# Kernel optimization log

Hardware: AMD Instinct MI355X
Metric: run time of the kernel (lower is better)

## Reference

```python
import jax, jax.numpy as jnp
import numpy as np

MARGIN = 1.0

def setup_inputs() -> dict:
    key = jax.random.key(0)
    k1, k2 = jax.random.split(key)
    B, D, NUM_CLASSES = 4096, 512, 64
    inputs = jax.random.normal(k1, (B, D), dtype=jnp.float32)
    labels = jax.random.randint(k2, (B,), 0, NUM_CLASSES, dtype=jnp.int64)
    return {"inputs": inputs, "labels": labels}

def reference(inputs, labels):
    # Full pairwise squared L2 distances via the ||a-b||^2 = ||a||^2 + ||b||^2 - 2 a.b expansion
    sq = jnp.sum(inputs * inputs, axis=1)                      # [B]
    d2 = sq[:, None] + sq[None, :] - 2.0 * (inputs @ inputs.T)  # [B, B]
    d2 = jnp.maximum(d2, 0.0)
    # Safe sqrt: zero (self) distances get exactly 0 without NaN-producing sqrt(0) grads
    nz = d2 > 1e-12
    dist = jnp.where(nz, jnp.sqrt(jnp.where(nz, d2, 1.0)), 0.0)  # [B, B]

    mask = labels[:, None] == labels[None, :]                   # [B, B] same-class mask (includes self)
    mask_f = mask.astype(dist.dtype)

    # Per-anchor: mean distance to positives (self included, contributing 0, as in the torch loop)
    ap_mean = jnp.sum(dist * mask_f, axis=1) / jnp.sum(mask_f, axis=1)  # [B]
    # Per-anchor: min distance to negatives
    an_min = jnp.min(jnp.where(mask, jnp.inf, dist), axis=1)            # [B]

    tmp = ap_mean - an_min + MARGIN                             # [B]
    # `if tmp > 0: loss += tmp` over the batch == sum of relu(tmp)
    return jnp.sum(jnp.maximum(tmp, 0.0))
```

## Files before the change

kernel.cpp:

```cpp
#include <hip/hip_runtime.h>
#include <hip/hip_bf16.h>

typedef unsigned char u8;
typedef unsigned short u16;
typedef unsigned int u32;
typedef unsigned long long u64;
typedef __attribute__((ext_vector_type(4))) float f32x4;

#define B_SZ 4096
#define D_SZ 512
#define NCLS 64
#define BK   64
#define NKK  (D_SZ / BK)
#define NT   32
#define NBLK (NT * (NT + 1) / 2)
#define TILE_BYTES (128 * BK)

#define WAITV2()  asm volatile("s_waitcnt vmcnt(2)" ::: "memory")
#define WAITV0()  asm volatile("s_waitcnt vmcnt(0)" ::: "memory")
#define BARRIER() asm volatile("s_barrier" ::: "memory")


__device__ __forceinline__ u8 f2fp8(float x) {
    union { float f; u32 u; } a; a.f = x;
    u32 s = (a.u >> 24) & 0x80u;
    u32 m = a.u & 0x7fffffffu;
    u32 r = m + 0x7ffffu + ((m >> 20) & 1u);
    int e = (int)(r >> 23) - 127 + 7;
    u32 mant = (r >> 20) & 7u;
    if (e <= 0) return (u8)s;
    if (e >= 16) return (u8)(s | 0x7Eu);
    return (u8)(s | ((u32)e << 3) | mant);
}

__device__ __forceinline__ void gload16(const void* g, void* l) {
    __builtin_amdgcn_global_load_lds(
        (const __attribute__((address_space(1))) u32*)g,
        (__attribute__((address_space(3))) u32*)l,
        16, 0, 0);
}

__device__ __forceinline__ void stage_fp8(const u8* __restrict__ gsrc, u8* dst, int t) {
    const int r = t >> 2;
    const int c16 = (t & 3) ^ (r & 3);
    gload16(gsrc + (size_t)r * D_SZ + (c16 << 4), dst + t * 16);
}


__global__ __launch_bounds__(256) void prep_kernel(
    const float* __restrict__ in, u8* __restrict__ bf8,
    float* __restrict__ sq, float* __restrict__ ap_sum, u32* __restrict__ an_min)
{
    const int wave = threadIdx.x >> 6, l = threadIdx.x & 63;
    const int row = blockIdx.x * 4 + wave;
    const float* p = in + (size_t)row * D_SZ + l * 8;
    float4 v0 = *(const float4*)p;
    float4 v1 = *(const float4*)(p + 4);
    float s = v0.x*v0.x + v0.y*v0.y + v0.z*v0.z + v0.w*v0.w
            + v1.x*v1.x + v1.y*v1.y + v1.z*v1.z + v1.w*v1.w;
    u64 pk =  (u64)f2fp8(v0.x)
           | ((u64)f2fp8(v0.y) << 8)
           | ((u64)f2fp8(v0.z) << 16)
           | ((u64)f2fp8(v0.w) << 24)
           | ((u64)f2fp8(v1.x) << 32)
           | ((u64)f2fp8(v1.y) << 40)
           | ((u64)f2fp8(v1.z) << 48)
           | ((u64)f2fp8(v1.w) << 56);
    *(u64*)(bf8 + (size_t)row * D_SZ + l * 8) = pk;
    #pragma unroll
    for (int off = 1; off < 64; off <<= 1) s += __shfl_xor(s, off);
    if (l == 0) {
        sq[row] = s;
        ap_sum[row] = 0.0f;
        an_min[row] = 0x7f800000u;
    }
}


__global__ __launch_bounds__(512, 4) void tile_kernel(
    const u8* __restrict__ bf8, const int* __restrict__ lab,
    const float* __restrict__ sq, float* __restrict__ ap_sum, u32* __restrict__ an_min)
{
    __shared__ u8 As[3][TILE_BYTES];
    __shared__ u8 Bs[3][TILE_BYTES];
    __shared__ float sqA[128], sqB[128];
    __shared__ int labA[128], labB[128];

    const int t = threadIdx.x;

    int bid = blockIdx.x;
    bid = (bid & 7) * (NBLK / 8) + (bid >> 3);

    int tm = (int)((__builtin_sqrtf(8.0f * (float)bid + 1.0f) - 1.0f) * 0.5f);
    while ((tm + 1) * (tm + 2) / 2 <= bid) ++tm;
    while (tm * (tm + 1) / 2 > bid) --tm;
    const int tn = bid - tm * (tm + 1) / 2;
    const bool diag = (tm == tn);

    const int rowBase = tm * 128;
    const int colBase = tn * 128;

    if (t < 128) { labA[t] = lab[rowBase + t]; sqA[t] = sq[rowBase + t]; }
    else if (t < 256) { int u = t - 128; labB[u] = lab[colBase + u]; sqB[u] = sq[colBase + u]; }

    const int wave = t >> 6, lane = t & 63;
    const int wr = wave >> 1, wc = wave & 1;
    const int g = lane >> 4, c = lane & 15;

    f32x4 acc[2][4];
    #pragma unroll
    for (int i = 0; i < 2; ++i)
        #pragma unroll
        for (int j = 0; j < 4; ++j)
            acc[i][j] = (f32x4){0.f, 0.f, 0.f, 0.f};

    const u8* gA = bf8 + (size_t)rowBase * D_SZ;
    const u8* gB = bf8 + (size_t)colBase * D_SZ;

    __syncthreads();

    stage_fp8(gA,      As[0], t);
    stage_fp8(gB,      Bs[0], t);
    stage_fp8(gA + BK, As[1], t);
    stage_fp8(gB + BK, Bs[1], t);

    const int x3 = c & 3, sub = (g & 1) * 8, gh = g >> 1;

    #pragma unroll
    for (int kk = 0; kk < NKK; ++kk) {
        if (kk < NKK - 1) { WAITV2(); }
        else              { WAITV0(); }
        BARRIER();

        if (kk + 2 < NKK) {
            stage_fp8(gA + (kk + 2) * BK, As[(kk + 2) % 3], t);
            stage_fp8(gB + (kk + 2) * BK, Bs[(kk + 2) % 3], t);
        }

        const u8* abuf = As[kk % 3];
        const u8* bbuf = Bs[kk % 3];

        #pragma unroll
        for (int ks = 0; ks < 2; ++ks) {
            const int koff = (((ks * 2 + gh) ^ x3) << 4) + sub;
            long a[2], b[4];
            #pragma unroll
            for (int mi = 0; mi < 2; ++mi)
                a[mi] = *(const long*)(abuf + (wr * 32 + mi * 16 + c) * BK + koff);
            #pragma unroll
            for (int ni = 0; ni < 4; ++ni)
                b[ni] = *(const long*)(bbuf + (wc * 64 + ni * 16 + c) * BK + koff);
            #pragma unroll
            for (int mi = 0; mi < 2; ++mi)
                #pragma unroll
                for (int ni = 0; ni < 4; ++ni)
                    acc[mi][ni] = __builtin_amdgcn_mfma_f32_16x16x32_fp8_fp8(a[mi], b[ni], acc[mi][ni], 0, 0, 0);
        }
    }

    float sc[4], mc[4];
    #pragma unroll
    for (int ni = 0; ni < 4; ++ni) { sc[ni] = 0.0f; mc[ni] = __builtin_inff(); }

    #pragma unroll
    for (int mi = 0; mi < 2; ++mi) {
        #pragma unroll
        for (int r = 0; r < 4; ++r) {
            const int lrow = wr * 32 + mi * 16 + g * 4 + r;
            const int i = rowBase + lrow;
            const int li = labA[lrow];
            const float sqi = sqA[lrow];
            float s = 0.0f;
            float mn = __builtin_inff();
            #pragma unroll
            for (int ni = 0; ni < 4; ++ni) {
                const int lcol = wc * 64 + ni * 16 + c;
                float d2 = sqi + sqB[lcol] - 2.0f * acc[mi][ni][r];
                d2 = fmaxf(d2, 0.0f);
                float dist = (d2 > 1e-12f) ? __builtin_sqrtf(d2) : 0.0f;
                if (diag && lrow == lcol) dist = 0.0f;
                if (li == labB[lcol]) { s += dist; sc[ni] += dist; }
                else                  { mn = fminf(mn, dist); mc[ni] = fminf(mc[ni], dist); }
            }
            #pragma unroll
            for (int off = 1; off < 16; off <<= 1) {
                s += __shfl_xor(s, off);
                mn = fminf(mn, __shfl_xor(mn, off));
            }
            if (c == 0) {
                atomicAdd(&ap_sum[i], s);
                atomicMin(&an_min[i], __float_as_uint(mn));
            }
        }
    }

    if (!diag) {
        #pragma unroll
        for (int ni = 0; ni < 4; ++ni) {
            float s = sc[ni], mn = mc[ni];
            s += __shfl_xor(s, 16); s += __shfl_xor(s, 32);
            mn = fminf(mn, __shfl_xor(mn, 16)); mn = fminf(mn, __shfl_xor(mn, 32));
            if (lane < 16) {
                const int j = colBase + wc * 64 + ni * 16 + c;
                atomicAdd(&ap_sum[j], s);
                atomicMin(&an_min[j], __float_as_uint(mn));
            }
        }
    }
}


__global__ __launch_bounds__(1024) void final_kernel(
    const float* __restrict__ ap_sum, const u32* __restrict__ an_min,
    const int* __restrict__ lab, float* __restrict__ out)
{
    __shared__ int cnt[NCLS];
    __shared__ float wsum[16];
    const int t = threadIdx.x;
    if (t < NCLS) cnt[t] = 0;
    __syncthreads();
    for (int i = t; i < B_SZ; i += 1024) atomicAdd(&cnt[lab[i]], 1);
    __syncthreads();
    float v = 0.0f;
    for (int i = t; i < B_SZ; i += 1024) {
        float apm = ap_sum[i] / (float)cnt[lab[i]];
        float anm = __uint_as_float(an_min[i]);
        v += fmaxf(apm - anm + 1.0f, 0.0f);
    }
    #pragma unroll
    for (int off = 1; off < 64; off <<= 1) v += __shfl_xor(v, off);
    if ((t & 63) == 0) wsum[t >> 6] = v;
    __syncthreads();
    if (t == 0) {
        float s = 0.0f;
        #pragma unroll
        for (int w = 0; w < 16; ++w) s += wsum[w];
        out[0] = s;
    }
}


extern "C" void kernel_launch(void* const* d_in, const int* in_sizes, int n_in,
                              void* d_out, int out_size, void* d_ws, size_t ws_size,
                              hipStream_t stream) {
    const float* inputs = (const float*)d_in[0];
    const int* labels = (const int*)d_in[1];
    float* out = (float*)d_out;

    char* ws = (char*)d_ws;
    float* ap_sum = (float*)ws;
    u32* an_min = (u32*)(ws + 16384);
    float* sq = (float*)(ws + 32768);
    u8* bf8 = (u8*)(ws + 65536);

    prep_kernel<<<dim3(B_SZ / 4), dim3(256), 0, stream>>>(inputs, bf8, sq, ap_sum, an_min);
    tile_kernel<<<dim3(NBLK), dim3(512), 0, stream>>>(bf8, labels, sq, ap_sum, an_min);
    final_kernel<<<dim3(1), dim3(1024), 0, stream>>>(ap_sum, an_min, labels, out);
}
```

Baseline: 45.05 us.

## Split each 128x128 distance tile into two 64-row blocks of 256 threads

Each triangular 128x128 tile is now handled by two 256-thread blocks, each covering 64 anchor rows against the full 128 columns, which doubles the grid size. The A stage shrinks to 64 rows while the B stage keeps 128 rows, loaded with two 16-byte loads per thread, and the wait count is adjusted to match. The self-distance check now compares global row and column indices. The aim is finer-grained work distribution and better load balance across CUs. The cost is that each B tile is loaded twice (more L2 traffic), and there are more atomics on the column-side reductions.

```diff
diff --git a/kernel.cpp b/kernel.cpp
--- a/kernel.cpp
+++ b/kernel.cpp
@@ -2,7 +2,6 @@
 #include <hip/hip_bf16.h>
 
 typedef unsigned char u8;
-typedef unsigned short u16;
 typedef unsigned int u32;
 typedef unsigned long long u64;
 typedef __attribute__((ext_vector_type(4))) float f32x4;
@@ -13,10 +12,12 @@
 #define BK   64
 #define NKK  (D_SZ / BK)
 #define NT   32
-#define NBLK (NT * (NT + 1) / 2)
-#define TILE_BYTES (128 * BK)
-
-#define WAITV2()  asm volatile("s_waitcnt vmcnt(2)" ::: "memory")
+#define NTILE (NT * (NT + 1) / 2)
+#define NBLK (NTILE * 2)
+#define A_BYTES (64 * BK)
+#define B_BYTES (128 * BK)
+
+#define WAITV3()  asm volatile("s_waitcnt vmcnt(3)" ::: "memory")
 #define WAITV0()  asm volatile("s_waitcnt vmcnt(0)" ::: "memory")
 #define BARRIER() asm volatile("s_barrier" ::: "memory")
 
@@ -40,10 +41,20 @@
         16, 0, 0);
 }
 
-__device__ __forceinline__ void stage_fp8(const u8* __restrict__ gsrc, u8* dst, int t) {
+__device__ __forceinline__ void stage_A(const u8* __restrict__ gsrc, u8* dst, int t) {
     const int r = t >> 2;
     const int c16 = (t & 3) ^ (r & 3);
     gload16(gsrc + (size_t)r * D_SZ + (c16 << 4), dst + t * 16);
+}
+
+__device__ __forceinline__ void stage_B(const u8* __restrict__ gsrc, u8* dst, int t) {
+    #pragma unroll
+    for (int q = 0; q < 2; ++q) {
+        const int s = t + q * 256;
+        const int r = s >> 2;
+        const int c16 = (s & 3) ^ (r & 3);
+        gload16(gsrc + (size_t)r * D_SZ + (c16 << 4), dst + s * 16);
+    }
 }
 
 
@@ -77,31 +88,33 @@
 }
 
 
-__global__ __launch_bounds__(512, 4) void tile_kernel(
+__global__ __launch_bounds__(256) void tile_kernel(
     const u8* __restrict__ bf8, const int* __restrict__ lab,
     const float* __restrict__ sq, float* __restrict__ ap_sum, u32* __restrict__ an_min)
 {
-    __shared__ u8 As[3][TILE_BYTES];
-    __shared__ u8 Bs[3][TILE_BYTES];
-    __shared__ float sqA[128], sqB[128];
-    __shared__ int labA[128], labB[128];
+    __shared__ u8 As[3][A_BYTES];
+    __shared__ u8 Bs[3][B_BYTES];
+    __shared__ float sqA[64], sqB[128];
+    __shared__ int labA[64], labB[128];
 
     const int t = threadIdx.x;
 
-    int bid = blockIdx.x;
-    bid = (bid & 7) * (NBLK / 8) + (bid >> 3);
-
-    int tm = (int)((__builtin_sqrtf(8.0f * (float)bid + 1.0f) - 1.0f) * 0.5f);
-    while ((tm + 1) * (tm + 2) / 2 <= bid) ++tm;
-    while (tm * (tm + 1) / 2 > bid) --tm;
-    const int tn = bid - tm * (tm + 1) / 2;
+    int b = blockIdx.x;
+    b = (b & 7) * (NBLK / 8) + (b >> 3);
+    const int tile = b >> 1;
+    const int half = b & 1;
+
+    int tm = (int)((__builtin_sqrtf(8.0f * (float)tile + 1.0f) - 1.0f) * 0.5f);
+    while ((tm + 1) * (tm + 2) / 2 <= tile) ++tm;
+    while (tm * (tm + 1) / 2 > tile) --tm;
+    const int tn = tile - tm * (tm + 1) / 2;
     const bool diag = (tm == tn);
 
-    const int rowBase = tm * 128;
+    const int rowBase = tm * 128 + half * 64;
     const int colBase = tn * 128;
 
-    if (t < 128) { labA[t] = lab[rowBase + t]; sqA[t] = sq[rowBase + t]; }
-    else if (t < 256) { int u = t - 128; labB[u] = lab[colBase + u]; sqB[u] = sq[colBase + u]; }
+    if (t < 64) { labA[t] = lab[rowBase + t]; sqA[t] = sq[rowBase + t]; }
+    else if (t < 192) { int u = t - 64; labB[u] = lab[colBase + u]; sqB[u] = sq[colBase + u]; }
 
     const int wave = t >> 6, lane = t & 63;
     const int wr = wave >> 1, wc = wave & 1;
@@ -119,22 +132,22 @@
 
     __syncthreads();
 
-    stage_fp8(gA,      As[0], t);
-    stage_fp8(gB,      Bs[0], t);
-    stage_fp8(gA + BK, As[1], t);
-    stage_fp8(gB + BK, Bs[1], t);
+    stage_A(gA,      As[0], t);
+    stage_B(gB,      Bs[0], t);
+    stage_A(gA + BK, As[1], t);
+    stage_B(gB + BK, Bs[1], t);
 
     const int x3 = c & 3, sub = (g & 1) * 8, gh = g >> 1;
 
     #pragma unroll
     for (int kk = 0; kk < NKK; ++kk) {
-        if (kk < NKK - 1) { WAITV2(); }
+        if (kk < NKK - 1) { WAITV3(); }
         else              { WAITV0(); }
         BARRIER();
 
         if (kk + 2 < NKK) {
-            stage_fp8(gA + (kk + 2) * BK, As[(kk + 2) % 3], t);
-            stage_fp8(gB + (kk + 2) * BK, Bs[(kk + 2) % 3], t);
+            stage_A(gA + (kk + 2) * BK, As[(kk + 2) % 3], t);
+            stage_B(gB + (kk + 2) * BK, Bs[(kk + 2) % 3], t);
         }
 
         const u8* abuf = As[kk % 3];
@@ -143,18 +156,18 @@
         #pragma unroll
         for (int ks = 0; ks < 2; ++ks) {
             const int koff = (((ks * 2 + gh) ^ x3) << 4) + sub;
-            long a[2], b[4];
+            long a[2], bfr[4];
             #pragma unroll
             for (int mi = 0; mi < 2; ++mi)
                 a[mi] = *(const long*)(abuf + (wr * 32 + mi * 16 + c) * BK + koff);
             #pragma unroll
             for (int ni = 0; ni < 4; ++ni)
-                b[ni] = *(const long*)(bbuf + (wc * 64 + ni * 16 + c) * BK + koff);
+                bfr[ni] = *(const long*)(bbuf + (wc * 64 + ni * 16 + c) * BK + koff);
             #pragma unroll
             for (int mi = 0; mi < 2; ++mi)
                 #pragma unroll
                 for (int ni = 0; ni < 4; ++ni)
-                    acc[mi][ni] = __builtin_amdgcn_mfma_f32_16x16x32_fp8_fp8(a[mi], b[ni], acc[mi][ni], 0, 0, 0);
+                    acc[mi][ni] = __builtin_amdgcn_mfma_f32_16x16x32_fp8_fp8(a[mi], bfr[ni], acc[mi][ni], 0, 0, 0);
         }
     }
 
@@ -175,10 +188,11 @@
             #pragma unroll
             for (int ni = 0; ni < 4; ++ni) {
                 const int lcol = wc * 64 + ni * 16 + c;
+                const int j = colBase + lcol;
                 float d2 = sqi + sqB[lcol] - 2.0f * acc[mi][ni][r];
                 d2 = fmaxf(d2, 0.0f);
                 float dist = (d2 > 1e-12f) ? __builtin_sqrtf(d2) : 0.0f;
-                if (diag && lrow == lcol) dist = 0.0f;
+                if (i == j) dist = 0.0f;
                 if (li == labB[lcol]) { s += dist; sc[ni] += dist; }
                 else                  { mn = fminf(mn, dist); mc[ni] = fminf(mc[ni], dist); }
             }
@@ -254,6 +268,6 @@
     u8* bf8 = (u8*)(ws + 65536);
 
     prep_kernel<<<dim3(B_SZ / 4), dim3(256), 0, stream>>>(inputs, bf8, sq, ap_sum, an_min);
-    tile_kernel<<<dim3(NBLK), dim3(512), 0, stream>>>(bf8, labels, sq, ap_sum, an_min);
+    tile_kernel<<<dim3(NBLK), dim3(256), 0, stream>>>(bf8, labels, sq, ap_sum, an_min);
     final_kernel<<<dim3(1), dim3(1024), 0, stream>>>(ap_sum, an_min, labels, out);
 }
```

Measured after the change: 42.34 us. -6.0%, faster.
